# Kernel tuning notes

Measured on AMD Instinct MI355X. Metric: run time of the kernel, lower is better.

The kernel has to match this reference:

```python
import jax, jax.numpy as jnp
import numpy as np

B, S, D, H = 2, 2048, 768, 12
DK = D // H


def setup_inputs() -> dict:
    key = jax.random.key(0)
    ks = jax.random.split(key, 10)
    sc = 0.02
    return {
        "k": jax.random.normal(ks[0], (B, S, D), jnp.float32),
        "q": jax.random.normal(ks[1], (B, S, D), jnp.float32),
        "v": jax.random.normal(ks[2], (B, S, D), jnp.float32),
        "mask": jnp.ones((B, 1, S, S), jnp.int32),
        "wq": jax.random.normal(ks[3], (D, D), jnp.float32) * sc,
        "bq": jnp.zeros((D,), jnp.float32),
        "wk": jax.random.normal(ks[4], (D, D), jnp.float32) * sc,
        "bk": jnp.zeros((D,), jnp.float32),
        "wv": jax.random.normal(ks[5], (D, D), jnp.float32) * sc,
        "bv": jnp.zeros((D,), jnp.float32),
        "wo": jax.random.normal(ks[6], (D, D), jnp.float32) * sc,
        "bo": jnp.zeros((D,), jnp.float32),
    }


def reference(k, q, v, mask, wq, bq, wk, bk, wv, bv, wo, bo):
    # Linear projections (torch Linear: x @ W^T + b)
    query = q @ wq.T + bq
    key_ = k @ wk.T + bk
    value = v @ wv.T + bv
    # [B,S,D] -> [B,H,S,DK]
    def split_heads(x):
        return x.reshape(B, S, H, DK).transpose(0, 2, 1, 3)
    Q, K, V = split_heads(query), split_heads(key_), split_heads(value)
    # NOTE: original masked_fill result is discarded -> mask is a no-op.
    scores = jnp.einsum("bhqd,bhkd->bhqk", Q, K) / jnp.sqrt(jnp.float32(DK))
    attn = jax.nn.softmax(scores, axis=-1)  # dropout p=0.0 -> identity
    out = jnp.einsum("bhqk,bhkd->bhqd", attn, V)
    out = out.transpose(0, 2, 1, 3).reshape(B, S, D)
    return out @ wo.T + bo
```

## Files before the change

kernel.cpp:

```cpp
#include <hip/hip_runtime.h>
#include <hip/hip_bf16.h>

#define B_  2
#define S_  2048
#define D_  768
#define H_  12
#define DK_ 64
#define NX_ (B_*S_*D_)
#define NW_ (D_*D_)
#define CSC 0.18033688011112042f

typedef __attribute__((ext_vector_type(8))) short  bf16x8;
typedef __attribute__((ext_vector_type(4))) float  f32x4;

__device__ __forceinline__ unsigned short f2bf(float f) {
    unsigned int u = __float_as_uint(f);
    u += 0x7fffu + ((u >> 16) & 1u);
    return (unsigned short)(u >> 16);
}

__device__ __forceinline__ unsigned cvtpk(float a, float b) {
    unsigned r;
    asm("v_cvt_pk_bf16_f32 %0, %1, %2" : "=v"(r) : "v"(a), "v"(b));
    return r;
}

__device__ __forceinline__ void async_cp16(const unsigned short* g,
                                           const unsigned short* lds_uniform_base) {
    __builtin_amdgcn_global_load_lds(
        (const __attribute__((address_space(1))) unsigned int*)(uintptr_t)g,
        (__attribute__((address_space(3))) unsigned int*)(unsigned int)(uintptr_t)lds_uniform_base,
        16, 0, 0);
}

struct CvtArgs { const float* s[7]; };

__global__ __launch_bounds__(256) void cvt_all(CvtArgs a,
                                               unsigned short* __restrict__ Xsw,
                                               unsigned short* __restrict__ Wsw) {
    const int bx = blockIdx.x;
    int y, inner;
    if (bx < 2304) { y = bx / 768;             inner = bx % 768; }
    else           { y = 3 + (bx - 2304) / 144; inner = (bx - 2304) % 144; }
    const int idx = inner * 256 + threadIdx.x;
    const int n  = idx / 48;
    const int g2 = idx % 48;
    const float* src = a.s[y] + (long)n * D_ + g2 * 16;
    const float zs = (y == 3) ? CSC : 1.0f;
    unsigned short o[16];
#pragma unroll
    for (int i = 0; i < 4; i++) {
        const float4 f = *(const float4*)(src + i * 4);
        o[i*4+0] = f2bf(f.x*zs); o[i*4+1] = f2bf(f.y*zs);
        o[i*4+2] = f2bf(f.z*zs); o[i*4+3] = f2bf(f.w*zs);
    }
    unsigned short* dst = (y >= 3) ? (Wsw + (long)(y - 3) * NW_ + (long)n * D_)
                                   : (Xsw + (long)y * NX_ + (long)n * D_);
    const int key = n & 7;
#pragma unroll
    for (int h = 0; h < 2; h++) {
        const int g8 = g2 * 2 + h;
        const int kdst = (g8 >> 3) * 64 + (((g8 & 7) ^ key) * 8);
        *(uint4*)(dst + kdst) = *(const uint4*)&o[h * 8];
    }
}

struct QkvArgs { const float* bias[3]; unsigned short* out[3]; };

__global__ __launch_bounds__(256, 3) void gemm_qkv(QkvArgs args,
                                                   const unsigned short* __restrict__ Xsw,
                                                   const unsigned short* __restrict__ Wsw) {
    __shared__ __align__(16) unsigned short smem[14336];
    unsigned short* As = smem;
    unsigned short* Bs = smem + 8192;

    const int t    = threadIdx.x;
    const int wave = t >> 6;
    const int lane = t & 63;
    const int l16  = lane & 15;
    const int quad = lane >> 4;
    const int wm   = wave >> 1, wn = wave & 1;
    const int m0   = blockIdx.x * 128;
    const int zz   = blockIdx.y >> 3;
    const int nb   = blockIdx.y & 7;
    const int n0   = nb * 96;

    const unsigned short* Ap = Xsw + (long)zz * NX_;
    const unsigned short* Wp = Wsw + (long)zz * NW_;

    f32x4 acc[4][3];
#pragma unroll
    for (int s = 0; s < 4; s++)
#pragma unroll
        for (int j = 0; j < 3; j++) acc[s][j] = (f32x4){0.f, 0.f, 0.f, 0.f};

    const int lrow = lane >> 3;
    const int lcg  = lane & 7;

    for (int k0 = 0; k0 < D_; k0 += 64) {
        __syncthreads();
#pragma unroll
        for (int i = 0; i < 4; i++) {
            const int chunk = wave * 4 + i;
            async_cp16(Ap + (long)(m0 + chunk * 8 + lrow) * D_ + k0 + lcg * 8,
                       As + chunk * 512);
        }
#pragma unroll
        for (int i = 0; i < 3; i++) {
            const int chunk = wave * 3 + i;
            async_cp16(Wp + (long)(n0 + chunk * 8 + lrow) * D_ + k0 + lcg * 8,
                       Bs + chunk * 512);
        }
        __syncthreads();
#pragma unroll
        for (int ks = 0; ks < 2; ks++) {
            const int cg = ks * 4 + quad;
            bf16x8 af[4], bf[3];
#pragma unroll
            for (int s = 0; s < 4; s++) {
                const int r = wm * 64 + s * 16 + l16;
                af[s] = *(const bf16x8*)&As[r * 64 + ((cg ^ (r & 7)) * 8)];
            }
#pragma unroll
            for (int j = 0; j < 3; j++) {
                const int r = wn * 48 + j * 16 + l16;
                bf[j] = *(const bf16x8*)&Bs[r * 64 + ((cg ^ (r & 7)) * 8)];
            }
#pragma unroll
            for (int s = 0; s < 4; s++)
#pragma unroll
                for (int j = 0; j < 3; j++)
                    acc[s][j] = __builtin_amdgcn_mfma_f32_16x16x32_bf16(af[s], bf[j], acc[s][j], 0, 0, 0);
        }
    }
    __syncthreads();

    const int b     = m0 >> 11;
    const int sbase = m0 & (S_ - 1);
    const float zs  = (zz == 0) ? CSC : 1.0f;
    float bv[3];
#pragma unroll
    for (int j = 0; j < 3; j++) bv[j] = args.bias[zz][n0 + wn * 48 + j * 16 + l16] * zs;

    if (zz < 2) {
        unsigned short* Ls = smem;
#pragma unroll
        for (int s = 0; s < 4; s++)
#pragma unroll
            for (int j = 0; j < 3; j++)
#pragma unroll
                for (int r = 0; r < 4; r++)
                    Ls[(wm * 64 + s * 16 + quad * 4 + r) * 104 + wn * 48 + j * 16 + l16] =
                        f2bf(acc[s][j][r] + bv[j]);
        __syncthreads();
        const int row  = t >> 1;
        const int half = t & 1;
        unsigned short* Op = args.out[zz];
#pragma unroll
        for (int i = 0; i < 6; i++) {
            const int colL = half * 48 + i * 8;
            const int gcol = n0 + colL;
            const int head = gcol >> 6;
            const int cih  = (gcol & 63) >> 3;
            const uint4 v = *(const uint4*)&Ls[row * 104 + colL];
            *(uint4*)(Op + ((long)(b * H_ + head) * S_ + sbase + row) * DK_
                         + ((cih ^ (row & 7)) * 8)) = v;
        }
    } else {
        unsigned short* Ls = smem;
#pragma unroll
        for (int s = 0; s < 4; s++)
#pragma unroll
            for (int j = 0; j < 3; j++)
#pragma unroll
                for (int r = 0; r < 4; r++) {
                    const int dkL = wn * 48 + j * 16 + l16;
                    const int pos = wm * 64 + (s >> 1) * 32 + quad * 8 + (s & 1) * 4 + r;
                    Ls[dkL * 136 + pos] = f2bf(acc[s][j][r] + bv[j]);
                }
        __syncthreads();
        unsigned short* Op = args.out[2];
#pragma unroll
        for (int e = 0; e < 6; e++) {
            const int idx = e * 256 + t;
            const int dkL = idx >> 4;
            const int c   = idx & 15;
            const int gdk  = n0 + dkL;
            const int head = gdk >> 6;
            const int dk   = gdk & 63;
            const uint4 v = *(const uint4*)&Ls[dkL * 136 + c * 8];
            *(uint4*)(Op + ((long)(b * H_ + head) * DK_ + dk) * S_
                         + sbase + (c >> 3) * 64 + (((c & 7) ^ (dk & 7)) * 8)) = v;
        }
    }
}

__global__ __launch_bounds__(256, 3) void attn_kernel(
    const unsigned short* __restrict__ Q, const unsigned short* __restrict__ K,
    const unsigned short* __restrict__ Vt, unsigned short* __restrict__ Ao)
{
    const int t    = threadIdx.x;
    const int wave = t >> 6;
    const int lane = t & 63;
    const int l16  = lane & 15;
    const int quad = lane >> 4;
    const int bid  = blockIdx.x;
    const int bh    = bid % 24;
    const int qtile = bid / 24;

    const unsigned short* Qp = Q  + (long)bh * S_ * DK_;
    const unsigned short* Kp = K  + (long)bh * S_ * DK_;
    const unsigned short* Vp = Vt + (long)bh * DK_ * S_;

    __shared__ __align__(16) unsigned short smem[16384];

    const int fkey = l16 & 7;
    const int fo0  = ((quad ^ fkey) * 8);
    const int fo1  = (((4 + quad) ^ fkey) * 8);

    bf16x8 qfrag[2];
    {
        const long qoff = (long)(qtile * 64 + wave * 16 + l16) * DK_;
        qfrag[0] = *(const bf16x8*)(Qp + qoff + fo0);
        qfrag[1] = *(const bf16x8*)(Qp + qoff + fo1);
    }

    const int ci0 = wave * 2;
    const int kd0 = ci0 * 512;
    const unsigned short* gk  = Kp + ci0 * 512 + lane * 8;
    const unsigned short* gv0 = Vp + (long)(ci0 * 8 + (lane >> 3)) * S_ + (lane & 7) * 8;
    const unsigned short* gv1 = gv0 + 8 * S_;

    async_cp16(gk,        smem + kd0);
    async_cp16(gk + 512,  smem + kd0 + 512);
    async_cp16(gv0,       smem + 8192 + kd0);
    async_cp16(gv1,       smem + 8192 + kd0 + 512);
    gk += 4096;  gv0 += 64;  gv1 += 64;

    f32x4 oacc[4];
#pragma unroll
    for (int j = 0; j < 4; j++) oacc[j] = (f32x4){0.f, 0.f, 0.f, 0.f};
    float lsum = 0.f;

    for (int it = 0; it < 32; ++it) {
        const int co = (it & 1) * 4096;
        const int no = 4096 - co;
        __syncthreads();
        const unsigned short* Ks = smem + co;
        const unsigned short* Vs = smem + 8192 + co;

        if (it < 31) {
            async_cp16(gk,        smem + no + kd0);
            async_cp16(gk + 512,  smem + no + kd0 + 512);
            async_cp16(gv0,       smem + 8192 + no + kd0);
            async_cp16(gv1,       smem + 8192 + no + kd0 + 512);
            gk += 4096;  gv0 += 64;  gv1 += 64;
        }

        f32x4 sacc[4];
#pragma unroll
        for (int j = 0; j < 4; j++) sacc[j] = (f32x4){0.f, 0.f, 0.f, 0.f};
#pragma unroll
        for (int ks = 0; ks < 2; ks++) {
            const int fo = ks ? fo1 : fo0;
            const bf16x8 qf = ks ? qfrag[1] : qfrag[0];
#pragma unroll
            for (int j = 0; j < 4; j++) {
                const bf16x8 bf = *(const bf16x8*)&Ks[(j * 16 + l16) * 64 + fo];
                sacc[j] = __builtin_amdgcn_mfma_f32_16x16x32_bf16(bf, qf, sacc[j], 0, 0, 0);
            }
        }

        float p[4][4];
#pragma unroll
        for (int j = 0; j < 4; j++)
#pragma unroll
            for (int r = 0; r < 4; r++)
                p[j][r] = exp2f(sacc[j][r]);
#pragma unroll
        for (int j = 0; j < 4; j++)
            lsum += (p[j][0] + p[j][1]) + (p[j][2] + p[j][3]);
        uint4 pw0, pw1;
        pw0.x = cvtpk(p[0][0], p[0][1]);  pw0.y = cvtpk(p[0][2], p[0][3]);
        pw0.z = cvtpk(p[1][0], p[1][1]);  pw0.w = cvtpk(p[1][2], p[1][3]);
        pw1.x = cvtpk(p[2][0], p[2][1]);  pw1.y = cvtpk(p[2][2], p[2][3]);
        pw1.z = cvtpk(p[3][0], p[3][1]);  pw1.w = cvtpk(p[3][2], p[3][3]);
        const bf16x8 pf0 = *(const bf16x8*)&pw0;
        const bf16x8 pf1 = *(const bf16x8*)&pw1;

#pragma unroll
        for (int ks = 0; ks < 2; ks++) {
            const int fo = ks ? fo1 : fo0;
            const bf16x8 pf = ks ? pf1 : pf0;
#pragma unroll
            for (int j = 0; j < 4; j++) {
                const bf16x8 vf = *(const bf16x8*)&Vs[(j * 16 + l16) * 64 + fo];
                oacc[j] = __builtin_amdgcn_mfma_f32_16x16x32_bf16(pf, vf, oacc[j], 0, 0, 0);
            }
        }
    }

    lsum += __shfl_xor(lsum, 16, 64);
    lsum += __shfl_xor(lsum, 32, 64);
    const float inv = 1.f / lsum;
    float scl[4];
#pragma unroll
    for (int r = 0; r < 4; r++) scl[r] = __shfl(inv, quad * 4 + r, 64);

    __syncthreads();
    unsigned short* Sc = smem;
#pragma unroll
    for (int j = 0; j < 4; j++)
#pragma unroll
        for (int r = 0; r < 4; r++) {
            const int row = wave * 16 + quad * 4 + r;
            const int c   = j * 2 + (l16 >> 3);
            Sc[row * 64 + ((c ^ (row & 7)) * 8) + (l16 & 7)] =
                f2bf(oacc[j][r] * scl[r]);
        }

    const int b = bh / H_, h = bh % H_;
    const int row = t >> 2;
    const int p0  = (t & 3) * 2;
    const int qrow = qtile * 64 + row;
    unsigned short* dst = Ao + (long)(b * S_ + qrow) * D_ + h * DK_;
    *(uint4*)(dst + p0 * 8)       = *(const uint4*)&Sc[row * 64 + p0 * 8];
    *(uint4*)(dst + (p0 + 1) * 8) = *(const uint4*)&Sc[row * 64 + (p0 + 1) * 8];
}

__global__ __launch_bounds__(256, 4) void gemm_out(
    const unsigned short* __restrict__ A, const unsigned short* __restrict__ Wsw,
    const float* __restrict__ bias, float* __restrict__ Out)
{
    __shared__ __align__(16) unsigned short smem[8704];
    unsigned short* As = smem;
    unsigned short* Bs = smem + 4096;

    const int t    = threadIdx.x;
    const int wave = t >> 6;
    const int lane = t & 63;
    const int l16  = lane & 15;
    const int quad = lane >> 4;
    const int wm   = wave >> 1, wn = wave & 1;
    const int m0   = blockIdx.x * 64;
    const int n0   = blockIdx.y * 64;

    f32x4 acc[2][2];
#pragma unroll
    for (int s = 0; s < 2; s++)
#pragma unroll
        for (int j = 0; j < 2; j++) acc[s][j] = (f32x4){0.f, 0.f, 0.f, 0.f};

    const int lrow = lane >> 3;
    const int lcg  = lane & 7;

    for (int k0 = 0; k0 < D_; k0 += 64) {
        __syncthreads();
#pragma unroll
        for (int i = 0; i < 2; i++) {
            const int chunk = wave * 2 + i;
            async_cp16(A + (long)(m0 + chunk * 8 + lrow) * D_ + k0 + lcg * 8,
                       As + chunk * 512);
        }
#pragma unroll
        for (int i = 0; i < 2; i++) {
            const int chunk = wave * 2 + i;
            async_cp16(Wsw + (long)(n0 + chunk * 8 + lrow) * D_ + k0 + lcg * 8,
                       Bs + chunk * 512);
        }
        __syncthreads();
#pragma unroll
        for (int ks = 0; ks < 2; ks++) {
            const int cg = ks * 4 + quad;
            bf16x8 af[2], bf[2];
#pragma unroll
            for (int s = 0; s < 2; s++) {
                const int r = wm * 32 + s * 16 + l16;
                af[s] = *(const bf16x8*)&As[r * 64 + ((cg ^ (r & 7)) * 8)];
            }
#pragma unroll
            for (int j = 0; j < 2; j++) {
                const int r = wn * 32 + j * 16 + l16;
                bf[j] = *(const bf16x8*)&Bs[r * 64 + ((cg ^ (r & 7)) * 8)];
            }
#pragma unroll
            for (int s = 0; s < 2; s++)
#pragma unroll
                for (int j = 0; j < 2; j++)
                    acc[s][j] = __builtin_amdgcn_mfma_f32_16x16x32_bf16(af[s], bf[j], acc[s][j], 0, 0, 0);
        }
    }

    float bv[2];
#pragma unroll
    for (int j = 0; j < 2; j++) bv[j] = bias[n0 + wn * 32 + j * 16 + l16];

    __syncthreads();
    float* fl = (float*)smem;
#pragma unroll
    for (int s = 0; s < 2; s++)
#pragma unroll
        for (int j = 0; j < 2; j++)
#pragma unroll
            for (int r = 0; r < 4; r++)
                fl[(wm * 32 + s * 16 + quad * 4 + r) * 67 + wn * 32 + j * 16 + l16] =
                    acc[s][j][r] + bv[j];
    __syncthreads();
    const int row = t >> 2, c0 = (t & 3) * 16;
#pragma unroll
    for (int i = 0; i < 4; i++) {
        const float4 v = *(const float4*)&fl[row * 67 + c0 + i * 4];
        *(float4*)(Out + (long)(m0 + row) * D_ + n0 + c0 + i * 4) = v;
    }
}

extern "C" void kernel_launch(void* const* d_in, const int* in_sizes, int n_in,
                              void* d_out, int out_size, void* d_ws, size_t ws_size,
                              hipStream_t stream) {
    const float* k_in = (const float*)d_in[0];
    const float* q_in = (const float*)d_in[1];
    const float* v_in = (const float*)d_in[2];
    const float* wq = (const float*)d_in[4];
    const float* bq = (const float*)d_in[5];
    const float* wk = (const float*)d_in[6];
    const float* bk = (const float*)d_in[7];
    const float* wv = (const float*)d_in[8];
    const float* bv = (const float*)d_in[9];
    const float* wo = (const float*)d_in[10];
    const float* bo = (const float*)d_in[11];

    unsigned short* ws = (unsigned short*)d_ws;
    unsigned short* Wsw = ws;
    unsigned short* Qb  = Wsw + 4ll * NW_;
    unsigned short* Kb  = Qb + (long)NX_;
    unsigned short* Vt  = Kb + (long)NX_;
    unsigned short* Xsw = Vt + (long)NX_;
    unsigned short* Ao  = Xsw;

    CvtArgs ca;
    ca.s[0] = q_in; ca.s[1] = k_in; ca.s[2] = v_in;
    ca.s[3] = wq;   ca.s[4] = wk;   ca.s[5] = wv;  ca.s[6] = wo;
    cvt_all<<<dim3(2880), 256, 0, stream>>>(ca, Xsw, Wsw);

    QkvArgs qa;
    qa.bias[0] = bq; qa.bias[1] = bk; qa.bias[2] = bv;
    qa.out[0] = Qb;  qa.out[1] = Kb;  qa.out[2] = Vt;
    gemm_qkv<<<dim3(32, 24), 256, 0, stream>>>(qa, Xsw, Wsw);

    attn_kernel<<<dim3(768), 256, 0, stream>>>(Qb, Kb, Vt, Ao);

    gemm_out<<<dim3(64, 12), 256, 0, stream>>>(Ao, Wsw + 3ll * NW_, bo, (float*)d_out);
}
```

Before: 202.2 us.

## Double-buffer LDS tiles in QKV and output GEMMs, retile QKV to one head

Both the QKV projection GEMM and the output GEMM now use two LDS buffers. The next K-slice is prefetched with async copies while MFMAs run on the current slice, which removes one barrier per iteration and hides global load latency. The QKV GEMM also moves from 128x96 to 128x64 tiles, so each block covers exactly one head. That simplifies the head-split epilogue and raises the grid to 36 columns of blocks. In exchange, LDS use per block roughly doubles, which may lower occupancy, and the smaller N tile reduces reuse of the A tile.

```diff
diff --git a/kernel.cpp b/kernel.cpp
--- a/kernel.cpp
+++ b/kernel.cpp
@@ -70,10 +70,7 @@
 __global__ __launch_bounds__(256, 3) void gemm_qkv(QkvArgs args,
                                                    const unsigned short* __restrict__ Xsw,
                                                    const unsigned short* __restrict__ Wsw) {
-    __shared__ __align__(16) unsigned short smem[14336];
-    unsigned short* As = smem;
-    unsigned short* Bs = smem + 8192;
-
+    __shared__ __align__(16) unsigned short smem[24576];
     const int t    = threadIdx.x;
     const int wave = t >> 6;
     const int lane = t & 63;
@@ -81,55 +78,74 @@
     const int quad = lane >> 4;
     const int wm   = wave >> 1, wn = wave & 1;
     const int m0   = blockIdx.x * 128;
-    const int zz   = blockIdx.y >> 3;
-    const int nb   = blockIdx.y & 7;
-    const int n0   = nb * 96;
+    const int zz   = blockIdx.y / 12;
+    const int nb   = blockIdx.y % 12;
+    const int n0   = nb * 64;
 
     const unsigned short* Ap = Xsw + (long)zz * NX_;
     const unsigned short* Wp = Wsw + (long)zz * NW_;
 
-    f32x4 acc[4][3];
+    f32x4 acc[4][2];
 #pragma unroll
     for (int s = 0; s < 4; s++)
 #pragma unroll
-        for (int j = 0; j < 3; j++) acc[s][j] = (f32x4){0.f, 0.f, 0.f, 0.f};
+        for (int j = 0; j < 2; j++) acc[s][j] = (f32x4){0.f, 0.f, 0.f, 0.f};
 
     const int lrow = lane >> 3;
     const int lcg  = lane & 7;
 
-    for (int k0 = 0; k0 < D_; k0 += 64) {
+#pragma unroll
+    for (int i = 0; i < 4; i++) {
+        const int chunk = wave * 4 + i;
+        async_cp16(Ap + (long)(m0 + chunk * 8 + lrow) * D_ + lcg * 8,
+                   smem + chunk * 512);
+    }
+#pragma unroll
+    for (int i = 0; i < 2; i++) {
+        const int chunk = wave * 2 + i;
+        async_cp16(Wp + (long)(n0 + chunk * 8 + lrow) * D_ + lcg * 8,
+                   smem + 8192 + chunk * 512);
+    }
+
+    for (int it = 0; it < 12; ++it) {
+        const int co = (it & 1) * 12288;
+        const int no = 12288 - co;
         __syncthreads();
-#pragma unroll
-        for (int i = 0; i < 4; i++) {
-            const int chunk = wave * 4 + i;
-            async_cp16(Ap + (long)(m0 + chunk * 8 + lrow) * D_ + k0 + lcg * 8,
-                       As + chunk * 512);
-        }
-#pragma unroll
-        for (int i = 0; i < 3; i++) {
-            const int chunk = wave * 3 + i;
-            async_cp16(Wp + (long)(n0 + chunk * 8 + lrow) * D_ + k0 + lcg * 8,
-                       Bs + chunk * 512);
-        }
-        __syncthreads();
+        if (it < 11) {
+            const int k1 = (it + 1) * 64;
+#pragma unroll
+            for (int i = 0; i < 4; i++) {
+                const int chunk = wave * 4 + i;
+                async_cp16(Ap + (long)(m0 + chunk * 8 + lrow) * D_ + k1 + lcg * 8,
+                           smem + no + chunk * 512);
+            }
+#pragma unroll
+            for (int i = 0; i < 2; i++) {
+                const int chunk = wave * 2 + i;
+                async_cp16(Wp + (long)(n0 + chunk * 8 + lrow) * D_ + k1 + lcg * 8,
+                           smem + no + 8192 + chunk * 512);
+            }
+        }
+        const unsigned short* As = smem + co;
+        const unsigned short* Bs = smem + co + 8192;
 #pragma unroll
         for (int ks = 0; ks < 2; ks++) {
             const int cg = ks * 4 + quad;
-            bf16x8 af[4], bf[3];
+            bf16x8 af[4], bf[2];
 #pragma unroll
             for (int s = 0; s < 4; s++) {
                 const int r = wm * 64 + s * 16 + l16;
                 af[s] = *(const bf16x8*)&As[r * 64 + ((cg ^ (r & 7)) * 8)];
             }
 #pragma unroll
-            for (int j = 0; j < 3; j++) {
-                const int r = wn * 48 + j * 16 + l16;
+            for (int j = 0; j < 2; j++) {
+                const int r = wn * 32 + j * 16 + l16;
                 bf[j] = *(const bf16x8*)&Bs[r * 64 + ((cg ^ (r & 7)) * 8)];
             }
 #pragma unroll
             for (int s = 0; s < 4; s++)
 #pragma unroll
-                for (int j = 0; j < 3; j++)
+                for (int j = 0; j < 2; j++)
                     acc[s][j] = __builtin_amdgcn_mfma_f32_16x16x32_bf16(af[s], bf[j], acc[s][j], 0, 0, 0);
         }
     }
@@ -138,32 +154,30 @@
     const int b     = m0 >> 11;
     const int sbase = m0 & (S_ - 1);
     const float zs  = (zz == 0) ? CSC : 1.0f;
-    float bv[3];
-#pragma unroll
-    for (int j = 0; j < 3; j++) bv[j] = args.bias[zz][n0 + wn * 48 + j * 16 + l16] * zs;
+    float bv[2];
+#pragma unroll
+    for (int j = 0; j < 2; j++) bv[j] = args.bias[zz][n0 + wn * 32 + j * 16 + l16] * zs;
 
     if (zz < 2) {
         unsigned short* Ls = smem;
 #pragma unroll
         for (int s = 0; s < 4; s++)
 #pragma unroll
-            for (int j = 0; j < 3; j++)
+            for (int j = 0; j < 2; j++)
 #pragma unroll
                 for (int r = 0; r < 4; r++)
-                    Ls[(wm * 64 + s * 16 + quad * 4 + r) * 104 + wn * 48 + j * 16 + l16] =
+                    Ls[(wm * 64 + s * 16 + quad * 4 + r) * 72 + wn * 32 + j * 16 + l16] =
                         f2bf(acc[s][j][r] + bv[j]);
         __syncthreads();
         const int row  = t >> 1;
         const int half = t & 1;
         unsigned short* Op = args.out[zz];
 #pragma unroll
-        for (int i = 0; i < 6; i++) {
-            const int colL = half * 48 + i * 8;
-            const int gcol = n0 + colL;
-            const int head = gcol >> 6;
-            const int cih  = (gcol & 63) >> 3;
-            const uint4 v = *(const uint4*)&Ls[row * 104 + colL];
-            *(uint4*)(Op + ((long)(b * H_ + head) * S_ + sbase + row) * DK_
+        for (int i = 0; i < 4; i++) {
+            const int col = half * 32 + i * 8;
+            const int cih = col >> 3;
+            const uint4 v = *(const uint4*)&Ls[row * 72 + col];
+            *(uint4*)(Op + ((long)(b * H_ + nb) * S_ + sbase + row) * DK_
                          + ((cih ^ (row & 7)) * 8)) = v;
         }
     } else {
@@ -171,25 +185,22 @@
 #pragma unroll
         for (int s = 0; s < 4; s++)
 #pragma unroll
-            for (int j = 0; j < 3; j++)
+            for (int j = 0; j < 2; j++)
 #pragma unroll
                 for (int r = 0; r < 4; r++) {
-                    const int dkL = wn * 48 + j * 16 + l16;
+                    const int dk  = wn * 32 + j * 16 + l16;
                     const int pos = wm * 64 + (s >> 1) * 32 + quad * 8 + (s & 1) * 4 + r;
-                    Ls[dkL * 136 + pos] = f2bf(acc[s][j][r] + bv[j]);
+                    Ls[dk * 136 + pos] = f2bf(acc[s][j][r] + bv[j]);
                 }
         __syncthreads();
         unsigned short* Op = args.out[2];
 #pragma unroll
-        for (int e = 0; e < 6; e++) {
+        for (int e = 0; e < 4; e++) {
             const int idx = e * 256 + t;
-            const int dkL = idx >> 4;
+            const int dk  = idx >> 4;
             const int c   = idx & 15;
-            const int gdk  = n0 + dkL;
-            const int head = gdk >> 6;
-            const int dk   = gdk & 63;
-            const uint4 v = *(const uint4*)&Ls[dkL * 136 + c * 8];
-            *(uint4*)(Op + ((long)(b * H_ + head) * DK_ + dk) * S_
+            const uint4 v = *(const uint4*)&Ls[dk * 136 + c * 8];
+            *(uint4*)(Op + ((long)(b * H_ + nb) * DK_ + dk) * S_
                          + sbase + (c >> 3) * 64 + (((c & 7) ^ (dk & 7)) * 8)) = v;
         }
     }
@@ -332,9 +343,7 @@
     const unsigned short* __restrict__ A, const unsigned short* __restrict__ Wsw,
     const float* __restrict__ bias, float* __restrict__ Out)
 {
-    __shared__ __align__(16) unsigned short smem[8704];
-    unsigned short* As = smem;
-    unsigned short* Bs = smem + 4096;
+    __shared__ __align__(16) unsigned short smem[16384];
 
     const int t    = threadIdx.x;
     const int wave = t >> 6;
@@ -354,21 +363,32 @@
     const int lrow = lane >> 3;
     const int lcg  = lane & 7;
 
-    for (int k0 = 0; k0 < D_; k0 += 64) {
+#pragma unroll
+    for (int i = 0; i < 2; i++) {
+        const int chunk = wave * 2 + i;
+        async_cp16(A + (long)(m0 + chunk * 8 + lrow) * D_ + lcg * 8,
+                   smem + chunk * 512);
+        async_cp16(Wsw + (long)(n0 + chunk * 8 + lrow) * D_ + lcg * 8,
+                   smem + 4096 + chunk * 512);
+    }
+
+    for (int it = 0; it < 12; ++it) {
+        const int co = (it & 1) * 8192;
+        const int no = 8192 - co;
         __syncthreads();
-#pragma unroll
-        for (int i = 0; i < 2; i++) {
-            const int chunk = wave * 2 + i;
-            async_cp16(A + (long)(m0 + chunk * 8 + lrow) * D_ + k0 + lcg * 8,
-                       As + chunk * 512);
-        }
-#pragma unroll
-        for (int i = 0; i < 2; i++) {
-            const int chunk = wave * 2 + i;
-            async_cp16(Wsw + (long)(n0 + chunk * 8 + lrow) * D_ + k0 + lcg * 8,
-                       Bs + chunk * 512);
-        }
-        __syncthreads();
+        if (it < 11) {
+            const int k1 = (it + 1) * 64;
+#pragma unroll
+            for (int i = 0; i < 2; i++) {
+                const int chunk = wave * 2 + i;
+                async_cp16(A + (long)(m0 + chunk * 8 + lrow) * D_ + k1 + lcg * 8,
+                           smem + no + chunk * 512);
+                async_cp16(Wsw + (long)(n0 + chunk * 8 + lrow) * D_ + k1 + lcg * 8,
+                           smem + no + 4096 + chunk * 512);
+            }
+        }
+        const unsigned short* As = smem + co;
+        const unsigned short* Bs = smem + co + 4096;
 #pragma unroll
         for (int ks = 0; ks < 2; ks++) {
             const int cg = ks * 4 + quad;
@@ -445,7 +465,7 @@
     QkvArgs qa;
     qa.bias[0] = bq; qa.bias[1] = bk; qa.bias[2] = bv;
     qa.out[0] = Qb;  qa.out[1] = Kb;  qa.out[2] = Vt;
-    gemm_qkv<<<dim3(32, 24), 256, 0, stream>>>(qa, Xsw, Wsw);
+    gemm_qkv<<<dim3(32, 36), 256, 0, stream>>>(qa, Xsw, Wsw);
 
     attn_kernel<<<dim3(768), 256, 0, stream>>>(Qb, Kb, Vt, Ao);
 
```

After: 200.8 us. No clear change (-0.7%).
